# Kernel optimization log

Hardware: AMD Instinct MI355X
Metric: run time of the kernel (lower is better)

Reference implementation:

```python
import jax, jax.numpy as jnp
import numpy as np

B, T, D = 32, 4096, 512  # batch, encoder timesteps t_k, attn_sz (== encoder dim == state_sz)


def setup_inputs() -> dict:
    key = jax.random.key(0)
    ks = jax.random.split(key, 7)
    scale = 1.0 / np.sqrt(D)
    return {
        "h_i": jax.random.normal(ks[0], (B, T, D), dtype=jnp.float32),
        "s_t": jax.random.normal(ks[1], (B, D), dtype=jnp.float32),
        "coverage": jax.random.uniform(ks[2], (B, T), dtype=jnp.float32),
        "W_h": jax.random.normal(ks[3], (D, D), dtype=jnp.float32) * scale,
        "W_s": jax.random.normal(ks[4], (D, D), dtype=jnp.float32) * scale,
        "b_s": jnp.zeros((D,), dtype=jnp.float32),
        "W_c": jax.random.normal(ks[5], (1, D), dtype=jnp.float32) * scale,
        "V": jax.random.normal(ks[6], (D, 1), dtype=jnp.float32) * scale,
    }


def reference(h_i, s_t, coverage, W_h, W_s, b_s, W_c, V):
    # enc_features: (B, T, D)
    enc_features = jnp.einsum("btd,de->bte", h_i, W_h)
    # dec_features: (B, D) broadcast over T
    dec_features = s_t @ W_s + b_s
    # coverage term: Dense(D) applied to coverage[..., None] -> outer product with W_c row
    cov_features = coverage[..., None] * W_c[0]  # (B, T, D)
    features = enc_features + dec_features[:, None, :] + cov_features
    # e_t = V(tanh(features)) squeezed to (B, T)
    e_t = jnp.einsum("bte,e->bt", jnp.tanh(features), V[:, 0])
    a_t = jax.nn.softmax(e_t, axis=1)  # (B, T)
    new_coverage = coverage + a_t
    # context = a_t^T h_i : (B, D)
    context_vector = jnp.einsum("bt,btd->bd", a_t, h_i)
    return context_vector, a_t, new_coverage
```

## Files before the change

kernel.cpp:

```cpp
#include <hip/hip_runtime.h>
#include <stdint.h>

#define B_ 32
#define T_ 4096
#define D_ 512
#define BT_ (B_*T_)
#define ROWS_ 128
#define NBLK_ (BT_/ROWS_)

typedef __attribute__((ext_vector_type(8))) short bf16x8;
typedef __attribute__((ext_vector_type(4))) float f32x4;

__device__ __forceinline__ unsigned short f2bf(float f) {
    unsigned int u = __float_as_uint(f);
    u += 0x7FFFu + ((u >> 16) & 1u);
    return (unsigned short)(u >> 16);
}

__device__ __forceinline__ unsigned pk2(float a, float b) {
    return (unsigned)f2bf(a) | ((unsigned)f2bf(b) << 16);
}

__device__ __forceinline__ float bf2f(unsigned short u) {
    return __uint_as_float(((unsigned)u) << 16);
}

__device__ __forceinline__ float tanh_fast(float x) {
    float e2 = __expf(2.0f * x);
    return 1.0f - 2.0f / (e2 + 1.0f);
}

__global__ __launch_bounds__(256) void k_conv_wh(const float* __restrict__ W_h,
                                                 unsigned short* __restrict__ wsb) {
    int tid = blockIdx.x * 256 + threadIdx.x;
    int l  = tid & 63;
    int kt = (tid >> 6) & 15;
    int nt = tid >> 10;
    int n  = nt * 16 + (l & 15);
    int k0 = kt * 32 + (l >> 4) * 8;
    unsigned int w[4];
#pragma unroll
    for (int q = 0; q < 4; ++q) {
        unsigned short lo = f2bf(W_h[(size_t)(k0 + 2*q)     * D_ + n]);
        unsigned short hi = f2bf(W_h[(size_t)(k0 + 2*q + 1) * D_ + n]);
        w[q] = (unsigned int)lo | ((unsigned int)hi << 16);
    }
    uint4 pk = {w[0], w[1], w[2], w[3]};
    ((uint4*)wsb)[tid] = pk;
}

__global__ __launch_bounds__(256) void k_dec(const float* __restrict__ s_t,
                                             const float* __restrict__ W_s,
                                             const float* __restrict__ b_s,
                                             float* __restrict__ dec) {
    int b = blockIdx.x;
    int c = threadIdx.x;
    float a0 = b_s[c], a1 = b_s[c + 256];
    const float* srow = s_t + b * D_;
    for (int k = 0; k < D_; ++k) {
        float s = srow[k];
        const float* wr = W_s + (size_t)k * D_;
        a0 = fmaf(s, wr[c], a0);
        a1 = fmaf(s, wr[c + 256], a1);
    }
    dec[b * D_ + c] = a0;
    dec[b * D_ + c + 256] = a1;
}

__global__ __launch_bounds__(1024, 4) void k_main(const float* __restrict__ h_i,
                                                  const float* __restrict__ coverage,
                                                  const unsigned short* __restrict__ wsb,
                                                  const float* __restrict__ dec,
                                                  const float* __restrict__ W_c,
                                                  const float* __restrict__ V,
                                                  float* __restrict__ e_out,
                                                  unsigned short* __restrict__ part) {
    __shared__ __align__(16) unsigned char As[131072];
    __shared__ float red[16][ROWS_];
    __shared__ float wexp[ROWS_];
    const int tid = threadIdx.x;
    const int w = tid >> 6, l = tid & 63;
    const int row0 = blockIdx.x * ROWS_;
    const int b    = row0 >> 12;
    const int t0   = row0 & (T_ - 1);

    {
        const int kt_s = l >> 2;
        const int lamf = ((l & 3) << 4) + w;
        const int slot = (lamf & 0x38) | ((lamf & 7) ^ ((l & 3) << 1) ^ (kt_s & 1));
        const int sb0  = (kt_s << 10) + (slot << 4);
        const float* gsrc = h_i + (size_t)(row0 + w) * D_ + l * 8;
#pragma unroll
        for (int p = 0; p < 8; ++p) {
            const float* src = gsrc + (size_t)(16 * p) * D_;
            float4 f0 = *(const float4*)src;
            float4 f1 = *(const float4*)(src + 4);
            uint4 pk;
            pk.x = pk2(f0.x, f0.y);
            pk.y = pk2(f0.z, f0.w);
            pk.z = pk2(f1.x, f1.y);
            pk.w = pk2(f1.z, f1.w);
            *(uint4*)(As + (p << 14) + sb0) = pk;
        }
    }
    __syncthreads();

    const int slotR = (l & 0x38) | ((l & 7) ^ (((l >> 4) & 3) << 1));
    const uint4* bw = (const uint4*)wsb + ((w * 2) << 10) + l;

    f32x4 acc[8][2];
#pragma unroll
    for (int af = 0; af < 8; ++af) {
        acc[af][0] = (f32x4){0, 0, 0, 0};
        acc[af][1] = (f32x4){0, 0, 0, 0};
    }

#pragma unroll
    for (int kt = 0; kt < 16; ++kt) {
        const int sl = (slotR ^ (kt & 1)) << 4;
        uint4 b0 = bw[(kt << 6)];
        uint4 b1 = bw[(1 << 10) + (kt << 6)];
#pragma unroll
        for (int af = 0; af < 8; ++af) {
            uint4 araw = *(const uint4*)(As + ((af * 16 + kt) << 10) + sl);
            bf16x8 a = __builtin_bit_cast(bf16x8, araw);
            acc[af][0] = __builtin_amdgcn_mfma_f32_16x16x32_bf16(
                a, __builtin_bit_cast(bf16x8, b0), acc[af][0], 0, 0, 0);
            acc[af][1] = __builtin_amdgcn_mfma_f32_16x16x32_bf16(
                a, __builtin_bit_cast(bf16x8, b1), acc[af][1], 0, 0, 0);
        }
    }

    const int rgrp = (l >> 4) * 4;
    {
        int col0 = w * 32 + (l & 15);
        float dv0 = dec[b * D_ + col0],      wc0 = W_c[col0],      vv0 = V[col0];
        float dv1 = dec[b * D_ + col0 + 16], wc1 = W_c[col0 + 16], vv1 = V[col0 + 16];
#pragma unroll
        for (int af = 0; af < 8; ++af) {
            float pr[4];
#pragma unroll
            for (int r = 0; r < 4; ++r) {
                float cv = coverage[b * T_ + t0 + af * 16 + rgrp + r];
                float x0 = acc[af][0][r] + dv0 + cv * wc0;
                float x1 = acc[af][1][r] + dv1 + cv * wc1;
                pr[r] = tanh_fast(x0) * vv0 + tanh_fast(x1) * vv1;
            }
#pragma unroll
            for (int mm = 1; mm <= 8; mm <<= 1)
#pragma unroll
                for (int r = 0; r < 4; ++r)
                    pr[r] += __shfl_xor(pr[r], mm, 64);
            if ((l & 15) == 0) {
#pragma unroll
                for (int r = 0; r < 4; ++r)
                    red[w][af * 16 + rgrp + r] = pr[r];
            }
        }
    }
    __syncthreads();
    if (tid < ROWS_) {
        float e = 0.f;
#pragma unroll
        for (int ww = 0; ww < 16; ++ww) e += red[ww][tid];
        e_out[b * T_ + t0 + tid] = e;
        wexp[tid] = __expf(e);
    }
    __syncthreads();

    {
        float pc[8] = {0, 0, 0, 0, 0, 0, 0, 0};
        const int sl = (slotR ^ (w & 1)) << 4;
#pragma unroll
        for (int af = 0; af < 8; ++af) {
            float wv = wexp[af * 16 + (l & 15)];
            uint4 araw = *(const uint4*)(As + ((af * 16 + w) << 10) + sl);
            const unsigned* u = (const unsigned*)&araw;
#pragma unroll
            for (int q = 0; q < 4; ++q) {
                float f0 = __uint_as_float(u[q] << 16);
                float f1 = __uint_as_float(u[q] & 0xffff0000u);
                pc[2 * q]     = fmaf(wv, f0, pc[2 * q]);
                pc[2 * q + 1] = fmaf(wv, f1, pc[2 * q + 1]);
            }
        }
#pragma unroll
        for (int mm = 1; mm <= 8; mm <<= 1)
#pragma unroll
            for (int j = 0; j < 8; ++j)
                pc[j] += __shfl_xor(pc[j], mm, 64);
        if ((l & 15) == 0) {
            unsigned short* dst = part + (size_t)blockIdx.x * D_ + w * 32 + (l >> 4) * 8;
            unsigned* d32 = (unsigned*)dst;
            d32[0] = pk2(pc[0], pc[1]);
            d32[1] = pk2(pc[2], pc[3]);
            d32[2] = pk2(pc[4], pc[5]);
            d32[3] = pk2(pc[6], pc[7]);
        }
    }
}

__global__ __launch_bounds__(256) void k_soft(const float* __restrict__ e_in,
                                              const float* __restrict__ coverage,
                                              float* __restrict__ out_at,
                                              float* __restrict__ out_cov,
                                              float* __restrict__ Sb) {
    int b = blockIdx.x, tid = threadIdx.x;
    __shared__ float red[4];
    float v[16];
    float m = -1e30f;
#pragma unroll
    for (int i = 0; i < 16; ++i) {
        v[i] = e_in[b * T_ + tid + i * 256];
        m = fmaxf(m, v[i]);
    }
#pragma unroll
    for (int mk = 1; mk <= 32; mk <<= 1) m = fmaxf(m, __shfl_xor(m, mk, 64));
    if ((tid & 63) == 0) red[tid >> 6] = m;
    __syncthreads();
    m = fmaxf(fmaxf(red[0], red[1]), fmaxf(red[2], red[3]));
    float s = 0.f;
#pragma unroll
    for (int i = 0; i < 16; ++i) { v[i] = expf(v[i] - m); s += v[i]; }
#pragma unroll
    for (int mk = 1; mk <= 32; mk <<= 1) s += __shfl_xor(s, mk, 64);
    __syncthreads();
    if ((tid & 63) == 0) red[tid >> 6] = s;
    __syncthreads();
    s = red[0] + red[1] + red[2] + red[3];
    if (tid == 0) Sb[b] = __expf(m) * s;
    float inv = 1.0f / s;
#pragma unroll
    for (int i = 0; i < 16; ++i) {
        int idx = b * T_ + tid + i * 256;
        float a = v[i] * inv;
        out_at[idx]  = a;
        out_cov[idx] = coverage[idx] + a;
    }
}

__global__ __launch_bounds__(256) void k_comb(const unsigned short* __restrict__ part,
                                              const float* __restrict__ Sb,
                                              float* __restrict__ out_ctx) {
    int idx = blockIdx.x * 256 + threadIdx.x;
    int b = idx >> 9, d = idx & 511;
    const unsigned short* pp = part + (size_t)b * 32 * D_ + d;
    float s = 0.f;
#pragma unroll 8
    for (int j = 0; j < 32; ++j) s += bf2f(pp[(size_t)j * D_]);
    out_ctx[idx] = s / Sb[b];
}

extern "C" void kernel_launch(void* const* d_in, const int* in_sizes, int n_in,
                              void* d_out, int out_size, void* d_ws, size_t ws_size,
                              hipStream_t stream) {
    const float* h_i      = (const float*)d_in[0];
    const float* s_t      = (const float*)d_in[1];
    const float* coverage = (const float*)d_in[2];
    const float* W_h      = (const float*)d_in[3];
    const float* W_s      = (const float*)d_in[4];
    const float* b_s      = (const float*)d_in[5];
    const float* W_c      = (const float*)d_in[6];
    const float* V        = (const float*)d_in[7];

    float* out_ctx = (float*)d_out;
    float* out_at  = out_ctx + B_ * D_;
    float* out_cov = out_at + BT_;

    unsigned short* wsb = (unsigned short*)d_ws;
    float* dec  = (float*)((char*)d_ws + 524288);
    unsigned short* part = (unsigned short*)(dec + B_ * D_);
    float* Sb   = (float*)(part + (size_t)NBLK_ * D_);

    k_conv_wh<<<128, 256, 0, stream>>>(W_h, wsb);
    k_dec<<<B_, 256, 0, stream>>>(s_t, W_s, b_s, dec);
    k_main<<<NBLK_, 1024, 0, stream>>>(h_i, coverage, wsb, dec, W_c, V, out_at, part);
    k_soft<<<B_, 256, 0, stream>>>(out_at, coverage, out_at, out_cov, Sb);
    k_comb<<<B_ * D_ / 256, 256, 0, stream>>>(part, Sb, out_ctx);
}
```

Measured before the change: 175.5 us.

## Pipeline main GEMM with triple-buffered global-to-LDS loads over K tiles

The main kernel drops the preload of the whole bf16 128x512 h tile into LDS. It now streams fp32 h and bf16 W_h K-tiles straight into LDS with global_load_lds, triple-buffered, so loads overlap the MFMA work. Blocks drop to 512 threads with a 2x4 warp tiling (4x8 MFMA tiles per warp), and A is converted to bf16 in registers. The context partial now rereads h_i from global in fp32 and stores fp32 partials. This adds a second pass over h_i, likely hitting L2, and raises register pressure.

```diff
diff --git a/kernel.cpp b/kernel.cpp
--- a/kernel.cpp
+++ b/kernel.cpp
@@ -21,14 +21,18 @@
     return (unsigned)f2bf(a) | ((unsigned)f2bf(b) << 16);
 }
 
-__device__ __forceinline__ float bf2f(unsigned short u) {
-    return __uint_as_float(((unsigned)u) << 16);
-}
-
 __device__ __forceinline__ float tanh_fast(float x) {
     float e2 = __expf(2.0f * x);
     return 1.0f - 2.0f / (e2 + 1.0f);
 }
+
+__device__ __forceinline__ void gl16(const void* g, const void* lds) {
+    __builtin_amdgcn_global_load_lds(
+        (const __attribute__((address_space(1))) void*)g,
+        (__attribute__((address_space(3))) void*)lds, 16, 0, 0);
+}
+
+#define WAITVM(N) asm volatile("s_waitcnt vmcnt(" #N ")" ::: "memory")
 
 __global__ __launch_bounds__(256) void k_conv_wh(const float* __restrict__ W_h,
                                                  unsigned short* __restrict__ wsb) {
@@ -67,84 +71,115 @@
     dec[b * D_ + c + 256] = a1;
 }
 
-__global__ __launch_bounds__(1024, 4) void k_main(const float* __restrict__ h_i,
-                                                  const float* __restrict__ coverage,
-                                                  const unsigned short* __restrict__ wsb,
-                                                  const float* __restrict__ dec,
-                                                  const float* __restrict__ W_c,
-                                                  const float* __restrict__ V,
-                                                  float* __restrict__ e_out,
-                                                  unsigned short* __restrict__ part) {
-    __shared__ __align__(16) unsigned char As[131072];
-    __shared__ float red[16][ROWS_];
+__global__ __launch_bounds__(512, 2) void k_main(const float* __restrict__ h_i,
+                                                 const float* __restrict__ coverage,
+                                                 const unsigned short* __restrict__ wsb,
+                                                 const float* __restrict__ dec,
+                                                 const float* __restrict__ W_c,
+                                                 const float* __restrict__ V,
+                                                 float* __restrict__ e_out,
+                                                 float* __restrict__ part) {
+    __shared__ __align__(16) unsigned char As[3 * 49152];
+    __shared__ float red[8][ROWS_];
     __shared__ float wexp[ROWS_];
     const int tid = threadIdx.x;
     const int w = tid >> 6, l = tid & 63;
+    const int m = w >> 2, n = w & 3;
     const int row0 = blockIdx.x * ROWS_;
     const int b    = row0 >> 12;
     const int t0   = row0 & (T_ - 1);
 
+    const float* gA = h_i + (size_t)(row0 + w * 16 + (l & 15)) * D_ + ((l >> 4) * 8);
+    const char*  gB = (const char*)wsb + w * 65536 + l * 16;
+
+#define STAGE(t, bp)  do {                                                    \
+        gl16(gA + (t) * 32,     (bp) + w * 2048);                             \
+        gl16(gA + (t) * 32 + 4, (bp) + w * 2048 + 1024);                      \
+        gl16(gB + 0 * 16384 + (t) * 1024, (bp) + 16384 + (w * 4 + 0) * 1024); \
+        gl16(gB + 1 * 16384 + (t) * 1024, (bp) + 16384 + (w * 4 + 1) * 1024); \
+        gl16(gB + 2 * 16384 + (t) * 1024, (bp) + 16384 + (w * 4 + 2) * 1024); \
+        gl16(gB + 3 * 16384 + (t) * 1024, (bp) + 16384 + (w * 4 + 3) * 1024); \
+    } while (0)
+
+    f32x4 acc[4][8];
+#pragma unroll
+    for (int af = 0; af < 4; ++af)
+#pragma unroll
+        for (int nt = 0; nt < 8; ++nt) acc[af][nt] = (f32x4){0, 0, 0, 0};
+
+    unsigned char* buf0 = As;
+    unsigned char* buf1 = As + 49152;
+    unsigned char* buf2 = As + 98304;
+
+#define COMPUTE(bp)  do {                                                     \
+        uint4 braw[8];                                                        \
+        _Pragma("unroll")                                                     \
+        for (int nt = 0; nt < 8; ++nt)                                        \
+            braw[nt] = *(const uint4*)((bp) + 16384 + (n * 8 + nt) * 1024 + l * 16); \
+        _Pragma("unroll")                                                     \
+        for (int af = 0; af < 4; ++af) {                                      \
+            const unsigned char* ab = (bp) + (m * 4 + af) * 2048 + l * 16;    \
+            float4 f0 = *(const float4*)ab;                                   \
+            float4 f1 = *(const float4*)(ab + 1024);                          \
+            uint4 a4 = {pk2(f0.x, f0.y), pk2(f0.z, f0.w),                     \
+                        pk2(f1.x, f1.y), pk2(f1.z, f1.w)};                    \
+            bf16x8 a = __builtin_bit_cast(bf16x8, a4);                        \
+            _Pragma("unroll")                                                 \
+            for (int nt = 0; nt < 8; ++nt)                                    \
+                acc[af][nt] = __builtin_amdgcn_mfma_f32_16x16x32_bf16(        \
+                    a, __builtin_bit_cast(bf16x8, braw[nt]), acc[af][nt], 0, 0, 0); \
+        }                                                                     \
+    } while (0)
+
+    STAGE(0, buf0);
+    STAGE(1, buf1);
+    WAITVM(6);
+    __builtin_amdgcn_s_barrier();
+    __builtin_amdgcn_sched_barrier(0);
+
     {
-        const int kt_s = l >> 2;
-        const int lamf = ((l & 3) << 4) + w;
-        const int slot = (lamf & 0x38) | ((lamf & 7) ^ ((l & 3) << 1) ^ (kt_s & 1));
-        const int sb0  = (kt_s << 10) + (slot << 4);
-        const float* gsrc = h_i + (size_t)(row0 + w) * D_ + l * 8;
-#pragma unroll
-        for (int p = 0; p < 8; ++p) {
-            const float* src = gsrc + (size_t)(16 * p) * D_;
-            float4 f0 = *(const float4*)src;
-            float4 f1 = *(const float4*)(src + 4);
-            uint4 pk;
-            pk.x = pk2(f0.x, f0.y);
-            pk.y = pk2(f0.z, f0.w);
-            pk.z = pk2(f1.x, f1.y);
-            pk.w = pk2(f1.z, f1.w);
-            *(uint4*)(As + (p << 14) + sb0) = pk;
+        unsigned char* bcur = buf0;
+        unsigned char* bnxt = buf1;
+        unsigned char* bstg = buf2;
+#pragma unroll 1
+        for (int t = 0; t < 14; ++t) {
+            STAGE(t + 2, bstg);
+            COMPUTE(bcur);
+            WAITVM(6);
+            __builtin_amdgcn_s_barrier();
+            __builtin_amdgcn_sched_barrier(0);
+            unsigned char* tmp = bcur; bcur = bnxt; bnxt = bstg; bstg = tmp;
         }
-    }
-    __syncthreads();
-
-    const int slotR = (l & 0x38) | ((l & 7) ^ (((l >> 4) & 3) << 1));
-    const uint4* bw = (const uint4*)wsb + ((w * 2) << 10) + l;
-
-    f32x4 acc[8][2];
-#pragma unroll
-    for (int af = 0; af < 8; ++af) {
-        acc[af][0] = (f32x4){0, 0, 0, 0};
-        acc[af][1] = (f32x4){0, 0, 0, 0};
-    }
-
-#pragma unroll
-    for (int kt = 0; kt < 16; ++kt) {
-        const int sl = (slotR ^ (kt & 1)) << 4;
-        uint4 b0 = bw[(kt << 6)];
-        uint4 b1 = bw[(1 << 10) + (kt << 6)];
-#pragma unroll
-        for (int af = 0; af < 8; ++af) {
-            uint4 araw = *(const uint4*)(As + ((af * 16 + kt) << 10) + sl);
-            bf16x8 a = __builtin_bit_cast(bf16x8, araw);
-            acc[af][0] = __builtin_amdgcn_mfma_f32_16x16x32_bf16(
-                a, __builtin_bit_cast(bf16x8, b0), acc[af][0], 0, 0, 0);
-            acc[af][1] = __builtin_amdgcn_mfma_f32_16x16x32_bf16(
-                a, __builtin_bit_cast(bf16x8, b1), acc[af][1], 0, 0, 0);
-        }
+        COMPUTE(bcur);
+        WAITVM(0);
+        __builtin_amdgcn_s_barrier();
+        __builtin_amdgcn_sched_barrier(0);
+        COMPUTE(bnxt);
     }
 
     const int rgrp = (l >> 4) * 4;
     {
-        int col0 = w * 32 + (l & 15);
-        float dv0 = dec[b * D_ + col0],      wc0 = W_c[col0],      vv0 = V[col0];
-        float dv1 = dec[b * D_ + col0 + 16], wc1 = W_c[col0 + 16], vv1 = V[col0 + 16];
-#pragma unroll
-        for (int af = 0; af < 8; ++af) {
+        float dv[8], wc8[8], vv8[8];
+#pragma unroll
+        for (int nt = 0; nt < 8; ++nt) {
+            int col = n * 128 + nt * 16 + (l & 15);
+            dv[nt]  = dec[b * D_ + col];
+            wc8[nt] = W_c[col];
+            vv8[nt] = V[col];
+        }
+#pragma unroll
+        for (int af = 0; af < 4; ++af) {
             float pr[4];
 #pragma unroll
             for (int r = 0; r < 4; ++r) {
-                float cv = coverage[b * T_ + t0 + af * 16 + rgrp + r];
-                float x0 = acc[af][0][r] + dv0 + cv * wc0;
-                float x1 = acc[af][1][r] + dv1 + cv * wc1;
-                pr[r] = tanh_fast(x0) * vv0 + tanh_fast(x1) * vv1;
+                float cv = coverage[b * T_ + t0 + m * 64 + af * 16 + rgrp + r];
+                float s = 0.f;
+#pragma unroll
+                for (int nt = 0; nt < 8; ++nt) {
+                    float x = acc[af][nt][r] + dv[nt] + cv * wc8[nt];
+                    s += tanh_fast(x) * vv8[nt];
+                }
+                pr[r] = s;
             }
 #pragma unroll
             for (int mm = 1; mm <= 8; mm <<= 1)
@@ -154,49 +189,50 @@
             if ((l & 15) == 0) {
 #pragma unroll
                 for (int r = 0; r < 4; ++r)
-                    red[w][af * 16 + rgrp + r] = pr[r];
+                    red[w][m * 64 + af * 16 + rgrp + r] = pr[r];
             }
         }
     }
     __syncthreads();
     if (tid < ROWS_) {
-        float e = 0.f;
-#pragma unroll
-        for (int ww = 0; ww < 16; ++ww) e += red[ww][tid];
+        int mg = tid >> 6;
+        float e = red[mg * 4 + 0][tid] + red[mg * 4 + 1][tid]
+                + red[mg * 4 + 2][tid] + red[mg * 4 + 3][tid];
         e_out[b * T_ + t0 + tid] = e;
         wexp[tid] = __expf(e);
     }
     __syncthreads();
 
     {
-        float pc[8] = {0, 0, 0, 0, 0, 0, 0, 0};
-        const int sl = (slotR ^ (w & 1)) << 4;
-#pragma unroll
-        for (int af = 0; af < 8; ++af) {
-            float wv = wexp[af * 16 + (l & 15)];
-            uint4 araw = *(const uint4*)(As + ((af * 16 + w) << 10) + sl);
-            const unsigned* u = (const unsigned*)&araw;
-#pragma unroll
-            for (int q = 0; q < 4; ++q) {
-                float f0 = __uint_as_float(u[q] << 16);
-                float f1 = __uint_as_float(u[q] & 0xffff0000u);
-                pc[2 * q]     = fmaf(wv, f0, pc[2 * q]);
-                pc[2 * q + 1] = fmaf(wv, f1, pc[2 * q + 1]);
-            }
+        const int rg = tid >> 7, dq = tid & 127;
+        const float* hb = h_i + (size_t)(row0 + rg * 32) * D_ + dq * 4;
+        float4 a0 = {0,0,0,0}, a1 = {0,0,0,0};
+#pragma unroll 4
+        for (int rr = 0; rr < 32; rr += 2) {
+            float w0 = wexp[rg * 32 + rr];
+            float w1 = wexp[rg * 32 + rr + 1];
+            float4 h0 = *(const float4*)(hb + (size_t)rr * D_);
+            float4 h1 = *(const float4*)(hb + (size_t)(rr + 1) * D_);
+            a0.x = fmaf(w0, h0.x, a0.x); a0.y = fmaf(w0, h0.y, a0.y);
+            a0.z = fmaf(w0, h0.z, a0.z); a0.w = fmaf(w0, h0.w, a0.w);
+            a1.x = fmaf(w1, h1.x, a1.x); a1.y = fmaf(w1, h1.y, a1.y);
+            a1.z = fmaf(w1, h1.z, a1.z); a1.w = fmaf(w1, h1.w, a1.w);
         }
-#pragma unroll
-        for (int mm = 1; mm <= 8; mm <<= 1)
-#pragma unroll
-            for (int j = 0; j < 8; ++j)
-                pc[j] += __shfl_xor(pc[j], mm, 64);
-        if ((l & 15) == 0) {
-            unsigned short* dst = part + (size_t)blockIdx.x * D_ + w * 32 + (l >> 4) * 8;
-            unsigned* d32 = (unsigned*)dst;
-            d32[0] = pk2(pc[0], pc[1]);
-            d32[1] = pk2(pc[2], pc[3]);
-            d32[2] = pk2(pc[4], pc[5]);
-            d32[3] = pk2(pc[6], pc[7]);
-        }
+        a0.x += a1.x; a0.y += a1.y; a0.z += a1.z; a0.w += a1.w;
+        float4* ctxred = (float4*)As;
+        ctxred[rg * 128 + dq] = a0;
+    }
+    __syncthreads();
+    if (tid < 128) {
+        const float4* ctxred = (const float4*)As;
+        float4 s0 = ctxred[tid], s1 = ctxred[128 + tid],
+               s2 = ctxred[256 + tid], s3 = ctxred[384 + tid];
+        float4 o;
+        o.x = (s0.x + s1.x) + (s2.x + s3.x);
+        o.y = (s0.y + s1.y) + (s2.y + s3.y);
+        o.z = (s0.z + s1.z) + (s2.z + s3.z);
+        o.w = (s0.w + s1.w) + (s2.w + s3.w);
+        *(float4*)(part + (size_t)blockIdx.x * D_ + tid * 4) = o;
     }
 }
 
@@ -239,15 +275,15 @@
     }
 }
 
-__global__ __launch_bounds__(256) void k_comb(const unsigned short* __restrict__ part,
+__global__ __launch_bounds__(256) void k_comb(const float* __restrict__ part,
                                               const float* __restrict__ Sb,
                                               float* __restrict__ out_ctx) {
     int idx = blockIdx.x * 256 + threadIdx.x;
     int b = idx >> 9, d = idx & 511;
-    const unsigned short* pp = part + (size_t)b * 32 * D_ + d;
+    const float* pp = part + (size_t)b * 32 * D_ + d;
     float s = 0.f;
 #pragma unroll 8
-    for (int j = 0; j < 32; ++j) s += bf2f(pp[(size_t)j * D_]);
+    for (int j = 0; j < 32; ++j) s += pp[(size_t)j * D_];
     out_ctx[idx] = s / Sb[b];
 }
 
@@ -269,12 +305,12 @@
 
     unsigned short* wsb = (unsigned short*)d_ws;
     float* dec  = (float*)((char*)d_ws + 524288);
-    unsigned short* part = (unsigned short*)(dec + B_ * D_);
-    float* Sb   = (float*)(part + (size_t)NBLK_ * D_);
+    float* part = dec + B_ * D_;
+    float* Sb   = part + (size_t)NBLK_ * D_;
 
     k_conv_wh<<<128, 256, 0, stream>>>(W_h, wsb);
     k_dec<<<B_, 256, 0, stream>>>(s_t, W_s, b_s, dec);
-    k_main<<<NBLK_, 1024, 0, stream>>>(h_i, coverage, wsb, dec, W_c, V, out_at, part);
+    k_main<<<NBLK_, 512, 0, stream>>>(h_i, coverage, wsb, dec, W_c, V, out_at, part);
     k_soft<<<B_, 256, 0, stream>>>(out_at, coverage, out_at, out_cov, Sb);
     k_comb<<<B_ * D_ / 256, 256, 0, stream>>>(part, Sb, out_ctx);
 }
```

After: 224.9 us. 1.28x slower.
